# Optimization experiments

Hardware: AMD Instinct MI355X
Metric: run time of the kernel (lower is better)

## Reference

```python
import jax, jax.numpy as jnp
import numpy as np


def _pairwise_iou(boxes):
    # boxes: [B, N, 4] in (x1, y1, x2, y2); returns IoU [B, N, N]
    area = (boxes[..., 2] - boxes[..., 0]) * (boxes[..., 3] - boxes[..., 1])  # [B, N]
    lt = jnp.maximum(boxes[:, :, None, :2], boxes[:, None, :, :2])  # [B, N, N, 2]
    rb = jnp.minimum(boxes[:, :, None, 2:], boxes[:, None, :, 2:])
    wh = jnp.clip(rb - lt, 0.0)
    inter = wh[..., 0] * wh[..., 1]  # [B, N, N]
    union = area[:, :, None] + area[:, None, :] - inter
    return inter / jnp.maximum(union, 1e-6)


def setup_inputs() -> dict:
    key = jax.random.key(0)
    kxy, kwh, ks = jax.random.split(key, 3)
    B, N, C = 4, 2048, 4
    xy = jax.random.uniform(kxy, (B, N, 2), dtype=jnp.float32) * 1000.0
    wh = jax.random.uniform(kwh, (B, N, 2), dtype=jnp.float32) * 100.0 + 1.0
    boxes = jnp.concatenate([xy, xy + wh], axis=-1)  # valid xyxy boxes
    scores = jax.random.uniform(ks, (B, C, N), dtype=jnp.float32)
    return {
        "boxes": boxes,
        "scores": scores,
        "iou_threshold": jnp.array([0.5], dtype=jnp.float32),
        "score_threshold": jnp.array([0.05], dtype=jnp.float32),
    }


def reference(boxes, scores, iou_threshold, score_threshold):
    # Greedy NMS-match (mmcv.ops.nms_match semantics), per batch and class.
    # Returns match: [B, C, N] int32 where match[b,c,n] is the index of the
    # group-leader (kept) box that box n belongs to, or -1 if unmatched
    # (i.e. score <= score_threshold).
    B, N, _ = boxes.shape
    C = scores.shape[1]
    thr = iou_threshold[0]
    sthr = score_threshold[0]

    iou = _pairwise_iou(boxes)  # [B, N, N] (shared across classes)
    order = jnp.argsort(-scores, axis=-1)  # [B, C, N], score-descending

    suppressed0 = scores <= sthr            # boxes below score threshold never match
    match0 = jnp.full((B, C, N), -1, jnp.int32)
    b_idx = jnp.arange(B)[:, None]          # [B, 1] for per-batch IoU row gather

    def step(carry, cand):
        # cand: [B, C] box index with next-highest score in each (batch, class)
        suppressed, match = carry           # [B, C, N] bool / int32
        cand_sup = jnp.take_along_axis(suppressed, cand[..., None], axis=-1)[..., 0]
        active = ~cand_sup                  # [B, C]: candidate not yet grouped
        cand_iou = iou[b_idx, cand]         # [B, C, N] IoU of candidate vs all boxes
        matched = active[..., None] & (~suppressed) & (cand_iou > thr)
        match = jnp.where(matched, cand[..., None].astype(jnp.int32), match)
        return (suppressed | matched, match), None

    xs = jnp.moveaxis(order, -1, 0)         # [N, B, C]: sequential greedy order
    (_, match), _ = jax.lax.scan(step, (suppressed0, match0), xs)
    return match
```

## Files before the change

### kernel.cpp

```cpp
#include <hip/hip_runtime.h>
#include <stdint.h>

#define N_   2048
#define NW   64
#define CLS  4
#define B_   4

__global__ __launch_bounds__(256) void build_mask(
    const float4* __restrict__ boxes, const float* __restrict__ thr_p,
    uint32_t* __restrict__ ov)
{
  __shared__ float4 sb[N_];
  const int b    = blockIdx.x >> 6;
  const int tile = blockIdx.x & 63;
  const float thr = thr_p[0];
  for (int i = threadIdx.x; i < N_; i += 256) sb[i] = boxes[b * N_ + i];
  __syncthreads();
  const int wv = threadIdx.x >> 6;
  const int ln = threadIdx.x & 63;
  #pragma unroll 2
  for (int rr = 0; rr < 8; ++rr) {
    const int r = tile * 32 + wv * 8 + rr;
    const float4 bi = sb[r];
    const float areai = (bi.z - bi.x) * (bi.w - bi.y);
    uint32_t myw = 0u;
    #pragma unroll 4
    for (int g = 0; g < 32; ++g) {
      const float4 bj = sb[g * 64 + ln];
      const float xx1 = fmaxf(bi.x, bj.x);
      const float yy1 = fmaxf(bi.y, bj.y);
      const float xx2 = fminf(bi.z, bj.z);
      const float yy2 = fminf(bi.w, bj.w);
      const float iw = fmaxf(xx2 - xx1, 0.0f);
      const float ih = fmaxf(yy2 - yy1, 0.0f);
      const float inter = iw * ih;
      const float areaj = (bj.z - bj.x) * (bj.w - bj.y);
      const float uni = fmaxf(areai + areaj - inter, 1e-6f);
      const unsigned long long bal = __ballot(inter / uni > thr);
      const uint32_t lo = (uint32_t)bal, hi = (uint32_t)(bal >> 32);
      if ((ln >> 1) == g) myw = (ln & 1) ? hi : lo;
    }
    ov[((size_t)(b * N_ + r)) * NW + ln] = myw;
  }
}


#define S_(r,c) \
  "v_and_b32 v35, v" #r ", v34\n\t"            \
  "v_cmp_ne_u32 vcc, 0, v35\n\t"               \
  "s_cmp_lg_u64 vcc, 0\n\t"                    \
  "s_cselect_b32 s40, 0, -1\n\t"               \
  "v_bfe_u32 v36, v" #c ", 5, 6\n\t"           \
  "v_cmp_eq_u32 s[42:43], v36, v32\n\t"        \
  "v_and_b32 v37, 31, v" #c "\n\t"             \
  "v_lshlrev_b32 v37, v37, v40\n\t"            \
  "v_cndmask_b32 v37, 0, v37, s[42:43]\n\t"    \
  "v_and_b32 v37, s40, v37\n\t"                \
  "v_or_b32 v34, v34, v37\n\t"

#define F_(r,c) \
  "v_lshlrev_b32 v38, 8, v" #c "\n\t"          \
  "v_add_u32 v38, v38, v33\n\t"                \
  "global_load_dword v" #r ", v38, %[B]\n\t"

#define PROC_A S_(92,44) S_(93,45) S_(94,46) S_(95,47) S_(96,48) S_(97,49) S_(98,50) S_(99,51) S_(100,52) S_(101,53) S_(102,54) S_(103,55) S_(104,56) S_(105,57) S_(106,58) S_(107,59)
#define PROC_B S_(108,60) S_(109,61) S_(110,62) S_(111,63) S_(112,64) S_(113,65) S_(114,66) S_(115,67) S_(116,68) S_(117,69) S_(118,70) S_(119,71) S_(120,72) S_(121,73) S_(122,74) S_(123,75)
#define PROC_C S_(124,76) S_(125,77) S_(126,78) S_(127,79) S_(128,80) S_(129,81) S_(130,82) S_(131,83) S_(132,84) S_(133,85) S_(134,86) S_(135,87) S_(136,88) S_(137,89) S_(138,90) S_(139,91)

#define REF_A F_(92,44) F_(93,45) F_(94,46) F_(95,47) F_(96,48) F_(97,49) F_(98,50) F_(99,51) F_(100,52) F_(101,53) F_(102,54) F_(103,55) F_(104,56) F_(105,57) F_(106,58) F_(107,59)
#define REF_B F_(108,60) F_(109,61) F_(110,62) F_(111,63) F_(112,64) F_(113,65) F_(114,66) F_(115,67) F_(116,68) F_(117,69) F_(118,70) F_(119,71) F_(120,72) F_(121,73) F_(122,74) F_(123,75)
#define REF_C F_(124,76) F_(125,77) F_(126,78) F_(127,79) F_(128,80) F_(129,81) F_(130,82) F_(131,83) F_(132,84) F_(133,85) F_(136,88) F_(134,86) F_(135,87) F_(137,89) F_(138,90) F_(139,91)

#define DSR_A \
  "ds_read_b128 v[44:47], v39\n\t"             \
  "ds_read_b128 v[48:51], v39 offset:16\n\t"   \
  "ds_read_b128 v[52:55], v39 offset:32\n\t"   \
  "ds_read_b128 v[56:59], v39 offset:48\n\t"   \
  "v_add_u32 v39, 64, v39\n\t"                 \
  "s_waitcnt lgkmcnt(0)\n\t"
#define DSR_B \
  "ds_read_b128 v[60:63], v39\n\t"             \
  "ds_read_b128 v[64:67], v39 offset:16\n\t"   \
  "ds_read_b128 v[68:71], v39 offset:32\n\t"   \
  "ds_read_b128 v[72:75], v39 offset:48\n\t"   \
  "v_add_u32 v39, 64, v39\n\t"                 \
  "s_waitcnt lgkmcnt(0)\n\t"
#define DSR_C \
  "ds_read_b128 v[76:79], v39\n\t"             \
  "ds_read_b128 v[80:83], v39 offset:16\n\t"   \
  "ds_read_b128 v[84:87], v39 offset:32\n\t"   \
  "ds_read_b128 v[88:91], v39 offset:48\n\t"   \
  "v_add_u32 v39, 64, v39\n\t"                 \
  "s_waitcnt lgkmcnt(0)\n\t"

__global__ __launch_bounds__(256, 1) void sort_scan(
    const float* __restrict__ scores, const float* __restrict__ sthr_p,
    const uint32_t* __restrict__ ov, int* __restrict__ match)
{
  __shared__ float sk[N_];
  __shared__ __align__(16) int sv[N_];
  __shared__ int rk[N_];
  __shared__ uint32_t sup0[NW];
  __shared__ uint32_t lead_s[NW];
  __shared__ int cnt_s;

  const int bc = blockIdx.x;
  const int b  = bc / CLS;
  const float sthr = sthr_p[0];
  const float* s = scores + (size_t)bc * N_;

  for (int i = threadIdx.x; i < N_; i += 256) {
    const float v = s[i];
    sk[i] = v;
    sv[i] = i;
    const unsigned long long bal = __ballot(v <= sthr);
    if ((threadIdx.x & 63) == 0) {
      sup0[(i >> 5)]     = (uint32_t)bal;
      sup0[(i >> 5) + 1] = (uint32_t)(bal >> 32);
    }
  }
  for (int size = 2; size <= N_; size <<= 1) {
    for (int stride = size >> 1; stride > 0; stride >>= 1) {
      __syncthreads();
      for (int t = threadIdx.x; t < N_ / 2; t += 256) {
        const int pos = 2 * t - (t & (stride - 1));
        const bool desc = ((t & (size >> 1)) == 0);
        const float ka = sk[pos], kb = sk[pos + stride];
        const int   va = sv[pos], vb = sv[pos + stride];
        const bool aBeforeB = (ka > kb) || (ka == kb && va < vb);
        if (desc != aBeforeB) {
          sk[pos] = kb; sk[pos + stride] = ka;
          sv[pos] = vb; sv[pos + stride] = va;
        }
      }
    }
  }
  __syncthreads();

  for (int i = threadIdx.x; i < N_; i += 256) rk[sv[i]] = i;
  if (threadIdx.x == 0) {
    int c = 0;
    for (int w = 0; w < NW; ++w) c += __popc(sup0[w]);
    cnt_s = N_ - c;
  }
  __syncthreads();
  {
    const int cnt = cnt_s;
    if (cnt > 0)
      for (int i = cnt + threadIdx.x; i < N_; i += 256) sv[i] = sv[cnt - 1];
  }
  __syncthreads();

  if (threadIdx.x < 64) {
    const int l  = threadIdx.x;
    const int l4 = l << 2;
    const uint32_t cb = (uint32_t)(uintptr_t)(&sv[0]);
    const uint32_t* rowb = ov + (size_t)b * N_ * NW;
    uint32_t vlead;
    asm volatile(
      "s_waitcnt vmcnt(0) lgkmcnt(0)\n\t"
      "v_mov_b32 v32, %[LN]\n\t"
      "v_mov_b32 v33, %[L4]\n\t"
      "v_mov_b32 v34, 0\n\t"
      "v_mov_b32 v39, %[CB]\n\t"
      "v_mov_b32 v40, 1\n\t"
      DSR_A REF_A
      DSR_B REF_B
      DSR_C REF_C
      "s_mov_b32 s41, 41\n\t"
      "LSCAN%=:\n\t"
      "s_waitcnt vmcnt(32)\n\t" PROC_A DSR_A REF_A
      "s_waitcnt vmcnt(32)\n\t" PROC_B DSR_B REF_B
      "s_waitcnt vmcnt(32)\n\t" PROC_C DSR_C REF_C
      "s_sub_u32 s41, s41, 1\n\t"
      "s_cmp_lg_u32 s41, 0\n\t"
      "s_cbranch_scc1 LSCAN%=\n\t"
      "s_waitcnt vmcnt(32)\n\t" PROC_A DSR_A REF_A
      "s_waitcnt vmcnt(32)\n\t" PROC_B DSR_B REF_B
      "s_waitcnt vmcnt(32)\n\t" PROC_C
      "s_waitcnt vmcnt(16)\n\t" PROC_A
      "s_waitcnt vmcnt(0)\n\t"  PROC_B
      "v_mov_b32 %[LD], v34\n\t"
      : [LD] "=v"(vlead)
      : [LN] "v"(l), [L4] "v"(l4), [CB] "v"(cb), [B] "s"(rowb)
      : "memory", "vcc", "scc", "s40", "s41", "s42", "s43",
        "v32","v33","v34","v35","v36","v37","v38","v39","v40","v41","v42","v43",
        "v44","v45","v46","v47","v48","v49","v50","v51","v52","v53","v54","v55",
        "v56","v57","v58","v59","v60","v61","v62","v63","v64","v65","v66","v67",
        "v68","v69","v70","v71","v72","v73","v74","v75","v76","v77","v78","v79",
        "v80","v81","v82","v83","v84","v85","v86","v87","v88","v89","v90","v91",
        "v92","v93","v94","v95","v96","v97","v98","v99","v100","v101","v102","v103",
        "v104","v105","v106","v107","v108","v109","v110","v111","v112","v113","v114","v115",
        "v116","v117","v118","v119","v120","v121","v122","v123","v124","v125","v126","v127",
        "v128","v129","v130","v131","v132","v133","v134","v135","v136","v137","v138","v139");
    lead_s[l] = vlead;
  }
  __syncthreads();

  const uint32_t* Mb = ov + (size_t)b * N_ * NW;
  for (int k = 0; k < 8; ++k) {
    const int n = (k << 8) + threadIdx.x;
    int res = -1;
    if (!((sup0[n >> 5] >> (n & 31)) & 1u)) {
      const uint4* r4 = (const uint4*)(Mb + (size_t)n * NW);
      const uint4* g4 = (const uint4*)lead_s;
      int best = 1 << 30;
      #pragma unroll
      for (int j = 0; j < 16; ++j) {
        const uint4 a = r4[j];
        const uint4 g = g4[j];
        uint32_t w0 = a.x & g.x, w1 = a.y & g.y, w2 = a.z & g.z, w3 = a.w & g.w;
        while (w0) { const int bb = __ffs(w0) - 1; w0 &= w0 - 1;
          const int jj = (j << 7) + bb;      const int r = rk[jj];
          if (r < best) { best = r; res = jj; } }
        while (w1) { const int bb = __ffs(w1) - 1; w1 &= w1 - 1;
          const int jj = (j << 7) + 32 + bb; const int r = rk[jj];
          if (r < best) { best = r; res = jj; } }
        while (w2) { const int bb = __ffs(w2) - 1; w2 &= w2 - 1;
          const int jj = (j << 7) + 64 + bb; const int r = rk[jj];
          if (r < best) { best = r; res = jj; } }
        while (w3) { const int bb = __ffs(w3) - 1; w3 &= w3 - 1;
          const int jj = (j << 7) + 96 + bb; const int r = rk[jj];
          if (r < best) { best = r; res = jj; } }
      }
    }
    match[(size_t)bc * N_ + n] = res;
  }
}

extern "C" void kernel_launch(void* const* d_in, const int* in_sizes, int n_in,
                              void* d_out, int out_size, void* d_ws, size_t ws_size,
                              hipStream_t stream)
{
  const float4* boxes  = (const float4*)d_in[0];
  const float*  scores = (const float*)d_in[1];
  const float*  iouthr = (const float*)d_in[2];
  const float*  scthr  = (const float*)d_in[3];
  int* match = (int*)d_out;

  uint32_t* ov = (uint32_t*)d_ws;

  build_mask<<<dim3(B_ * 64),  dim3(256), 0, stream>>>(boxes, iouthr, ov);
  sort_scan <<<dim3(B_ * CLS), dim3(256), 0, stream>>>(scores, scthr, ov, match);
}
```

Baseline: 227.8 us.

## Overlap score sort with mask build and restructure scan to precompute bit masks

Moves the per-class bitonic sort out of the serial scan kernel into extra blocks of the mask-building launch, so the sort runs concurrently with IoU mask construction. The sort now uses packed 64-bit keys (score bits plus inverted index) and writes order, rank and suppression words to workspace. The mask kernel computes 8 rows per wave at once to reuse each loaded neighbour box. The inline-asm greedy scan now prefetches order indices into separate registers and precomputes lane bit masks alongside each load, shortening the per-candidate dependency chain. In exchange it adds extra workspace traffic and a global reload of order and rank in the second kernel.

```diff
diff --git a/kernel.cpp b/kernel.cpp
--- a/kernel.cpp
+++ b/kernel.cpp
@@ -5,149 +5,191 @@
 #define NW   64
 #define CLS  4
 #define B_   4
-
-__global__ __launch_bounds__(256) void build_mask(
+#define ORD_STRIDE (N_ + 64)
+
+__global__ __launch_bounds__(256) void mask_or_sort(
     const float4* __restrict__ boxes, const float* __restrict__ thr_p,
-    uint32_t* __restrict__ ov)
+    const float* __restrict__ scores, const float* __restrict__ sthr_p,
+    uint32_t* __restrict__ ov, int* __restrict__ order,
+    int* __restrict__ rk, uint32_t* __restrict__ sup0ws)
 {
-  __shared__ float4 sb[N_];
-  const int b    = blockIdx.x >> 6;
-  const int tile = blockIdx.x & 63;
-  const float thr = thr_p[0];
-  for (int i = threadIdx.x; i < N_; i += 256) sb[i] = boxes[b * N_ + i];
-  __syncthreads();
-  const int wv = threadIdx.x >> 6;
-  const int ln = threadIdx.x & 63;
-  #pragma unroll 2
-  for (int rr = 0; rr < 8; ++rr) {
-    const int r = tile * 32 + wv * 8 + rr;
-    const float4 bi = sb[r];
-    const float areai = (bi.z - bi.x) * (bi.w - bi.y);
-    uint32_t myw = 0u;
-    #pragma unroll 4
+  __shared__ __align__(16) unsigned char lds_raw[32768];
+  __shared__ uint32_t sup_l[NW];
+  __shared__ int cnt_s;
+
+  if (blockIdx.x < 256) {
+    float4* sb = (float4*)lds_raw;
+    const int b    = blockIdx.x >> 6;
+    const int tile = blockIdx.x & 63;
+    const float thr = thr_p[0];
+    for (int i = threadIdx.x; i < N_; i += 256) sb[i] = boxes[b * N_ + i];
+    __syncthreads();
+    const int wv = threadIdx.x >> 6;
+    const int ln = threadIdx.x & 63;
+    const int r0 = tile * 32 + wv * 8;
+    float4 bi[8]; float areai[8];
+    #pragma unroll
+    for (int rr = 0; rr < 8; ++rr) {
+      bi[rr] = sb[r0 + rr];
+      areai[rr] = (bi[rr].z - bi[rr].x) * (bi[rr].w - bi[rr].y);
+    }
+    uint32_t myw[8] = {0, 0, 0, 0, 0, 0, 0, 0};
     for (int g = 0; g < 32; ++g) {
       const float4 bj = sb[g * 64 + ln];
-      const float xx1 = fmaxf(bi.x, bj.x);
-      const float yy1 = fmaxf(bi.y, bj.y);
-      const float xx2 = fminf(bi.z, bj.z);
-      const float yy2 = fminf(bi.w, bj.w);
-      const float iw = fmaxf(xx2 - xx1, 0.0f);
-      const float ih = fmaxf(yy2 - yy1, 0.0f);
-      const float inter = iw * ih;
       const float areaj = (bj.z - bj.x) * (bj.w - bj.y);
-      const float uni = fmaxf(areai + areaj - inter, 1e-6f);
-      const unsigned long long bal = __ballot(inter / uni > thr);
-      const uint32_t lo = (uint32_t)bal, hi = (uint32_t)(bal >> 32);
-      if ((ln >> 1) == g) myw = (ln & 1) ? hi : lo;
-    }
-    ov[((size_t)(b * N_ + r)) * NW + ln] = myw;
+      const bool sel = ((ln >> 1) == g);
+      const bool hi  = (ln & 1);
+      #pragma unroll
+      for (int rr = 0; rr < 8; ++rr) {
+        const float xx1 = fmaxf(bi[rr].x, bj.x);
+        const float yy1 = fmaxf(bi[rr].y, bj.y);
+        const float xx2 = fminf(bi[rr].z, bj.z);
+        const float yy2 = fminf(bi[rr].w, bj.w);
+        const float iw = fmaxf(xx2 - xx1, 0.0f);
+        const float ih = fmaxf(yy2 - yy1, 0.0f);
+        const float inter = iw * ih;
+        const float uni = fmaxf(areai[rr] + areaj - inter, 1e-6f);
+        const unsigned long long bal = __ballot(inter / uni > thr);
+        const uint32_t w = hi ? (uint32_t)(bal >> 32) : (uint32_t)bal;
+        if (sel) myw[rr] = w;
+      }
+    }
+    #pragma unroll
+    for (int rr = 0; rr < 8; ++rr)
+      ov[((size_t)(b * N_ + r0 + rr)) * NW + ln] = myw[rr];
+  } else {
+    unsigned long long* sp = (unsigned long long*)lds_raw;
+    const int bc = blockIdx.x - 256;
+    const float sthr = sthr_p[0];
+    const float* s = scores + (size_t)bc * N_;
+    for (int i = threadIdx.x; i < N_; i += 256) {
+      const float v = s[i];
+      uint32_t u = __float_as_uint(v);
+      u = (u >> 31) ? ~u : (u | 0x80000000u);
+      sp[i] = ((unsigned long long)u << 32) | (uint32_t)(~(uint32_t)i);
+      const unsigned long long bal = __ballot(v <= sthr);
+      if ((threadIdx.x & 63) == 0) {
+        sup_l[(i >> 5)]     = (uint32_t)bal;
+        sup_l[(i >> 5) + 1] = (uint32_t)(bal >> 32);
+      }
+    }
+    for (int size = 2; size <= N_; size <<= 1) {
+      for (int stride = size >> 1; stride > 0; stride >>= 1) {
+        __syncthreads();
+        for (int t = threadIdx.x; t < N_ / 2; t += 256) {
+          const int pos = 2 * t - (t & (stride - 1));
+          const bool desc = ((t & (size >> 1)) == 0);
+          const unsigned long long a = sp[pos], c = sp[pos + stride];
+          if (desc != (a > c)) { sp[pos] = c; sp[pos + stride] = a; }
+        }
+      }
+    }
+    __syncthreads();
+    if (threadIdx.x == 0) {
+      int c2 = 0;
+      for (int w = 0; w < NW; ++w) c2 += __popc(sup_l[w]);
+      cnt_s = N_ - c2;
+    }
+    __syncthreads();
+    const int cnt = cnt_s;
+    const int last = (cnt > 0) ? (int)~(uint32_t)sp[cnt - 1] : 0;
+    int* ord_o = order + (size_t)bc * ORD_STRIDE;
+    int* rk_o  = rk    + (size_t)bc * N_;
+    for (int i = threadIdx.x; i < N_; i += 256) {
+      const int idx = (int)~(uint32_t)sp[i];
+      ord_o[i] = (i < cnt || cnt == 0) ? idx : last;
+      rk_o[idx] = i;
+    }
+    for (int i = N_ + threadIdx.x; i < ORD_STRIDE; i += 256) ord_o[i] = last;
+    if (threadIdx.x < NW) sup0ws[bc * NW + threadIdx.x] = sup_l[threadIdx.x];
   }
 }
 
 
-#define S_(r,c) \
-  "v_and_b32 v35, v" #r ", v34\n\t"            \
+#define S6_(rw,bt) \
+  "v_and_b32 v35, v" #rw ", v34\n\t"           \
   "v_cmp_ne_u32 vcc, 0, v35\n\t"               \
   "s_cmp_lg_u64 vcc, 0\n\t"                    \
   "s_cselect_b32 s40, 0, -1\n\t"               \
-  "v_bfe_u32 v36, v" #c ", 5, 6\n\t"           \
+  "v_and_b32 v37, s40, v" #bt "\n\t"           \
+  "v_or_b32 v34, v34, v37\n\t"
+
+#define RF_(rw,st) \
+  "v_lshlrev_b32 v38, 8, v" #st "\n\t"         \
+  "v_add_u32 v38, v38, v33\n\t"                \
+  "global_load_dword v" #rw ", v38, %[B]\n\t"
+
+#define MB_(bt,st) \
+  "v_bfe_u32 v36, v" #st ", 5, 6\n\t"          \
   "v_cmp_eq_u32 s[42:43], v36, v32\n\t"        \
-  "v_and_b32 v37, 31, v" #c "\n\t"             \
-  "v_lshlrev_b32 v37, v37, v40\n\t"            \
-  "v_cndmask_b32 v37, 0, v37, s[42:43]\n\t"    \
-  "v_and_b32 v37, s40, v37\n\t"                \
-  "v_or_b32 v34, v34, v37\n\t"
-
-#define F_(r,c) \
-  "v_lshlrev_b32 v38, 8, v" #c "\n\t"          \
-  "v_add_u32 v38, v38, v33\n\t"                \
-  "global_load_dword v" #r ", v38, %[B]\n\t"
-
-#define PROC_A S_(92,44) S_(93,45) S_(94,46) S_(95,47) S_(96,48) S_(97,49) S_(98,50) S_(99,51) S_(100,52) S_(101,53) S_(102,54) S_(103,55) S_(104,56) S_(105,57) S_(106,58) S_(107,59)
-#define PROC_B S_(108,60) S_(109,61) S_(110,62) S_(111,63) S_(112,64) S_(113,65) S_(114,66) S_(115,67) S_(116,68) S_(117,69) S_(118,70) S_(119,71) S_(120,72) S_(121,73) S_(122,74) S_(123,75)
-#define PROC_C S_(124,76) S_(125,77) S_(126,78) S_(127,79) S_(128,80) S_(129,81) S_(130,82) S_(131,83) S_(132,84) S_(133,85) S_(134,86) S_(135,87) S_(136,88) S_(137,89) S_(138,90) S_(139,91)
-
-#define REF_A F_(92,44) F_(93,45) F_(94,46) F_(95,47) F_(96,48) F_(97,49) F_(98,50) F_(99,51) F_(100,52) F_(101,53) F_(102,54) F_(103,55) F_(104,56) F_(105,57) F_(106,58) F_(107,59)
-#define REF_B F_(108,60) F_(109,61) F_(110,62) F_(111,63) F_(112,64) F_(113,65) F_(114,66) F_(115,67) F_(116,68) F_(117,69) F_(118,70) F_(119,71) F_(120,72) F_(121,73) F_(122,74) F_(123,75)
-#define REF_C F_(124,76) F_(125,77) F_(126,78) F_(127,79) F_(128,80) F_(129,81) F_(130,82) F_(131,83) F_(132,84) F_(133,85) F_(136,88) F_(134,86) F_(135,87) F_(137,89) F_(138,90) F_(139,91)
-
-#define DSR_A \
-  "ds_read_b128 v[44:47], v39\n\t"             \
-  "ds_read_b128 v[48:51], v39 offset:16\n\t"   \
-  "ds_read_b128 v[52:55], v39 offset:32\n\t"   \
-  "ds_read_b128 v[56:59], v39 offset:48\n\t"   \
-  "v_add_u32 v39, 64, v39\n\t"                 \
-  "s_waitcnt lgkmcnt(0)\n\t"
-#define DSR_B \
-  "ds_read_b128 v[60:63], v39\n\t"             \
-  "ds_read_b128 v[64:67], v39 offset:16\n\t"   \
-  "ds_read_b128 v[68:71], v39 offset:32\n\t"   \
-  "ds_read_b128 v[72:75], v39 offset:48\n\t"   \
-  "v_add_u32 v39, 64, v39\n\t"                 \
-  "s_waitcnt lgkmcnt(0)\n\t"
-#define DSR_C \
-  "ds_read_b128 v[76:79], v39\n\t"             \
-  "ds_read_b128 v[80:83], v39 offset:16\n\t"   \
-  "ds_read_b128 v[84:87], v39 offset:32\n\t"   \
-  "ds_read_b128 v[88:91], v39 offset:48\n\t"   \
-  "v_add_u32 v39, 64, v39\n\t"                 \
-  "s_waitcnt lgkmcnt(0)\n\t"
-
-__global__ __launch_bounds__(256, 1) void sort_scan(
-    const float* __restrict__ scores, const float* __restrict__ sthr_p,
-    const uint32_t* __restrict__ ov, int* __restrict__ match)
+  "v_cndmask_b32 v37, 0, v40, s[42:43]\n\t"    \
+  "v_lshlrev_b32 v" #bt ", v" #st ", v37\n\t"
+
+#define CAND(rw,bt,st) S6_(rw,bt) RF_(rw,st) MB_(bt,st)
+#define CP(rw,bt,st)   RF_(rw,st) MB_(bt,st)
+
+#define DSR4 \
+  "ds_read_b128 v[140:143], v39\n\t"           \
+  "ds_read_b128 v[144:147], v39 offset:16\n\t" \
+  "ds_read_b128 v[148:151], v39 offset:32\n\t" \
+  "ds_read_b128 v[152:155], v39 offset:48\n\t" \
+  "v_add_u32 v39, 64, v39\n\t"
+
+#define PH_HDR "s_waitcnt vmcnt(32)\n\t" "s_waitcnt lgkmcnt(0)\n\t"
+
+#define PH_A PH_HDR \
+  CAND(92,44,140)  CAND(93,45,141)  CAND(94,46,142)  CAND(95,47,143)  \
+  CAND(96,48,144)  CAND(97,49,145)  CAND(98,50,146)  CAND(99,51,147)  \
+  CAND(100,52,148) CAND(101,53,149) CAND(102,54,150) CAND(103,55,151) \
+  CAND(104,56,152) CAND(105,57,153) CAND(106,58,154) CAND(107,59,155) DSR4
+#define PH_B PH_HDR \
+  CAND(108,60,140) CAND(109,61,141) CAND(110,62,142) CAND(111,63,143) \
+  CAND(112,64,144) CAND(113,65,145) CAND(114,66,146) CAND(115,67,147) \
+  CAND(116,68,148) CAND(117,69,149) CAND(118,70,150) CAND(119,71,151) \
+  CAND(120,72,152) CAND(121,73,153) CAND(122,74,154) CAND(123,75,155) DSR4
+#define PH_C PH_HDR \
+  CAND(124,76,140) CAND(125,77,141) CAND(126,78,142) CAND(127,79,143) \
+  CAND(128,80,144) CAND(129,81,145) CAND(130,82,146) CAND(131,83,147) \
+  CAND(132,84,148) CAND(133,85,149) CAND(134,86,150) CAND(135,87,151) \
+  CAND(136,88,152) CAND(137,89,153) CAND(138,90,154) CAND(139,91,155) DSR4
+
+#define PRO_A \
+  CP(92,44,140)  CP(93,45,141)  CP(94,46,142)  CP(95,47,143)  \
+  CP(96,48,144)  CP(97,49,145)  CP(98,50,146)  CP(99,51,147)  \
+  CP(100,52,148) CP(101,53,149) CP(102,54,150) CP(103,55,151) \
+  CP(104,56,152) CP(105,57,153) CP(106,58,154) CP(107,59,155)
+#define PRO_B \
+  CP(108,60,140) CP(109,61,141) CP(110,62,142) CP(111,63,143) \
+  CP(112,64,144) CP(113,65,145) CP(114,66,146) CP(115,67,147) \
+  CP(116,68,148) CP(117,69,149) CP(118,70,150) CP(119,71,151) \
+  CP(120,72,152) CP(121,73,153) CP(122,74,154) CP(123,75,155)
+#define PRO_C \
+  CP(124,76,140) CP(125,77,141) CP(126,78,142) CP(127,79,143) \
+  CP(128,80,144) CP(129,81,145) CP(130,82,146) CP(131,83,147) \
+  CP(132,84,148) CP(133,85,149) CP(134,86,150) CP(135,87,151) \
+  CP(136,88,152) CP(137,89,153) CP(138,90,154) CP(139,91,155)
+
+__global__ __launch_bounds__(256, 1) void scan_extract(
+    const uint32_t* __restrict__ ov, const int* __restrict__ order,
+    const int* __restrict__ rk, const uint32_t* __restrict__ sup0ws,
+    int* __restrict__ match)
 {
-  __shared__ float sk[N_];
-  __shared__ __align__(16) int sv[N_];
-  __shared__ int rk[N_];
-  __shared__ uint32_t sup0[NW];
+  __shared__ __align__(16) int sv[ORD_STRIDE];
+  __shared__ __align__(16) int rk_s[N_];
   __shared__ uint32_t lead_s[NW];
-  __shared__ int cnt_s;
+  __shared__ uint32_t sup_s[NW];
 
   const int bc = blockIdx.x;
   const int b  = bc / CLS;
-  const float sthr = sthr_p[0];
-  const float* s = scores + (size_t)bc * N_;
-
-  for (int i = threadIdx.x; i < N_; i += 256) {
-    const float v = s[i];
-    sk[i] = v;
-    sv[i] = i;
-    const unsigned long long bal = __ballot(v <= sthr);
-    if ((threadIdx.x & 63) == 0) {
-      sup0[(i >> 5)]     = (uint32_t)bal;
-      sup0[(i >> 5) + 1] = (uint32_t)(bal >> 32);
-    }
-  }
-  for (int size = 2; size <= N_; size <<= 1) {
-    for (int stride = size >> 1; stride > 0; stride >>= 1) {
-      __syncthreads();
-      for (int t = threadIdx.x; t < N_ / 2; t += 256) {
-        const int pos = 2 * t - (t & (stride - 1));
-        const bool desc = ((t & (size >> 1)) == 0);
-        const float ka = sk[pos], kb = sk[pos + stride];
-        const int   va = sv[pos], vb = sv[pos + stride];
-        const bool aBeforeB = (ka > kb) || (ka == kb && va < vb);
-        if (desc != aBeforeB) {
-          sk[pos] = kb; sk[pos + stride] = ka;
-          sv[pos] = vb; sv[pos + stride] = va;
-        }
-      }
-    }
-  }
-  __syncthreads();
-
-  for (int i = threadIdx.x; i < N_; i += 256) rk[sv[i]] = i;
-  if (threadIdx.x == 0) {
-    int c = 0;
-    for (int w = 0; w < NW; ++w) c += __popc(sup0[w]);
-    cnt_s = N_ - c;
-  }
-  __syncthreads();
+
   {
-    const int cnt = cnt_s;
-    if (cnt > 0)
-      for (int i = cnt + threadIdx.x; i < N_; i += 256) sv[i] = sv[cnt - 1];
+    const int4* osrc = (const int4*)(order + (size_t)bc * ORD_STRIDE);
+    int4* odst = (int4*)sv;
+    for (int i = threadIdx.x; i < ORD_STRIDE / 4; i += 256) odst[i] = osrc[i];
+    const int4* rsrc = (const int4*)(rk + (size_t)bc * N_);
+    int4* rdst = (int4*)rk_s;
+    for (int i = threadIdx.x; i < N_ / 4; i += 256) rdst[i] = rsrc[i];
+    if (threadIdx.x < NW) sup_s[threadIdx.x] = sup0ws[bc * NW + threadIdx.x];
   }
   __syncthreads();
 
@@ -164,22 +206,18 @@
       "v_mov_b32 v34, 0\n\t"
       "v_mov_b32 v39, %[CB]\n\t"
       "v_mov_b32 v40, 1\n\t"
-      DSR_A REF_A
-      DSR_B REF_B
-      DSR_C REF_C
-      "s_mov_b32 s41, 41\n\t"
+      DSR4 "s_waitcnt lgkmcnt(0)\n\t" PRO_A
+      DSR4 "s_waitcnt lgkmcnt(0)\n\t" PRO_B
+      DSR4 "s_waitcnt lgkmcnt(0)\n\t" PRO_C
+      DSR4
+      "s_mov_b32 s41, 42\n\t"
       "LSCAN%=:\n\t"
-      "s_waitcnt vmcnt(32)\n\t" PROC_A DSR_A REF_A
-      "s_waitcnt vmcnt(32)\n\t" PROC_B DSR_B REF_B
-      "s_waitcnt vmcnt(32)\n\t" PROC_C DSR_C REF_C
+      PH_A PH_B PH_C
       "s_sub_u32 s41, s41, 1\n\t"
       "s_cmp_lg_u32 s41, 0\n\t"
       "s_cbranch_scc1 LSCAN%=\n\t"
-      "s_waitcnt vmcnt(32)\n\t" PROC_A DSR_A REF_A
-      "s_waitcnt vmcnt(32)\n\t" PROC_B DSR_B REF_B
-      "s_waitcnt vmcnt(32)\n\t" PROC_C
-      "s_waitcnt vmcnt(16)\n\t" PROC_A
-      "s_waitcnt vmcnt(0)\n\t"  PROC_B
+      PH_A PH_B
+      "s_waitcnt vmcnt(0) lgkmcnt(0)\n\t"
       "v_mov_b32 %[LD], v34\n\t"
       : [LD] "=v"(vlead)
       : [LN] "v"(l), [L4] "v"(l4), [CB] "v"(cb), [B] "s"(rowb)
@@ -192,7 +230,9 @@
         "v92","v93","v94","v95","v96","v97","v98","v99","v100","v101","v102","v103",
         "v104","v105","v106","v107","v108","v109","v110","v111","v112","v113","v114","v115",
         "v116","v117","v118","v119","v120","v121","v122","v123","v124","v125","v126","v127",
-        "v128","v129","v130","v131","v132","v133","v134","v135","v136","v137","v138","v139");
+        "v128","v129","v130","v131","v132","v133","v134","v135","v136","v137","v138","v139",
+        "v140","v141","v142","v143","v144","v145","v146","v147","v148","v149","v150","v151",
+        "v152","v153","v154","v155");
     lead_s[l] = vlead;
   }
   __syncthreads();
@@ -201,7 +241,7 @@
   for (int k = 0; k < 8; ++k) {
     const int n = (k << 8) + threadIdx.x;
     int res = -1;
-    if (!((sup0[n >> 5] >> (n & 31)) & 1u)) {
+    if (!((sup_s[n >> 5] >> (n & 31)) & 1u)) {
       const uint4* r4 = (const uint4*)(Mb + (size_t)n * NW);
       const uint4* g4 = (const uint4*)lead_s;
       int best = 1 << 30;
@@ -211,16 +251,16 @@
         const uint4 g = g4[j];
         uint32_t w0 = a.x & g.x, w1 = a.y & g.y, w2 = a.z & g.z, w3 = a.w & g.w;
         while (w0) { const int bb = __ffs(w0) - 1; w0 &= w0 - 1;
-          const int jj = (j << 7) + bb;      const int r = rk[jj];
+          const int jj = (j << 7) + bb;      const int r = rk_s[jj];
           if (r < best) { best = r; res = jj; } }
         while (w1) { const int bb = __ffs(w1) - 1; w1 &= w1 - 1;
-          const int jj = (j << 7) + 32 + bb; const int r = rk[jj];
+          const int jj = (j << 7) + 32 + bb; const int r = rk_s[jj];
           if (r < best) { best = r; res = jj; } }
         while (w2) { const int bb = __ffs(w2) - 1; w2 &= w2 - 1;
-          const int jj = (j << 7) + 64 + bb; const int r = rk[jj];
+          const int jj = (j << 7) + 64 + bb; const int r = rk_s[jj];
           if (r < best) { best = r; res = jj; } }
         while (w3) { const int bb = __ffs(w3) - 1; w3 &= w3 - 1;
-          const int jj = (j << 7) + 96 + bb; const int r = rk[jj];
+          const int jj = (j << 7) + 96 + bb; const int r = rk_s[jj];
           if (r < best) { best = r; res = jj; } }
       }
     }
@@ -238,8 +278,14 @@
   const float*  scthr  = (const float*)d_in[3];
   int* match = (int*)d_out;
 
-  uint32_t* ov = (uint32_t*)d_ws;
-
-  build_mask<<<dim3(B_ * 64),  dim3(256), 0, stream>>>(boxes, iouthr, ov);
-  sort_scan <<<dim3(B_ * CLS), dim3(256), 0, stream>>>(scores, scthr, ov, match);
+  char* ws = (char*)d_ws;
+  uint32_t* ov    = (uint32_t*)ws;
+  int*      order = (int*)(ws + (size_t)B_ * N_ * NW * 4);
+  int*      rk    = (int*)((char*)order + (size_t)B_ * CLS * ORD_STRIDE * 4);
+  uint32_t* sup0  = (uint32_t*)((char*)rk + (size_t)B_ * CLS * N_ * 4);
+
+  mask_or_sort<<<dim3(256 + B_ * CLS), dim3(256), 0, stream>>>(
+      boxes, iouthr, scores, scthr, ov, order, rk, sup0);
+  scan_extract<<<dim3(B_ * CLS), dim3(256), 0, stream>>>(
+      ov, order, rk, sup0, match);
 }
```

After: 203.5 us. -10.7%, faster.
